# Kernel optimization log

Hardware: AMD Instinct MI355X
Metric: run time of the kernel (lower is better)

## Reference

```python
import jax, jax.numpy as jnp
import numpy as np
from math import pi

EPS = 1e-7
GAIN = 3.5  # weight_logits_softmax_gain
MAX_LOG_VAR = 3.5


def _upper_triangular(v, T, K, D):
    # replicate tf concat([v, v[...,::-1], zeros[...,D]], axis=2) -> reshape [T,K,D,D] -> strict-upper mask
    zero_pad = jnp.zeros((T, K, D), dtype=v.dtype)
    a_flat = jnp.concatenate([v, v[..., ::-1], zero_pad], axis=2)
    a = a_flat.reshape(T, K, D, D)
    idx = jnp.arange(D)
    mask = (idx[:, None] < idx[None, :]).astype(v.dtype)
    return a * mask[None, None, :, :]


def _diag_transforms(cov_param, T, K, D):
    ut = _upper_triangular(cov_param, T, K, D)
    a = 0.5 * (jnp.swapaxes(ut, -1, -2) - ut)  # antisymmetric [T,K,D,D]
    eye = jnp.eye(D, dtype=cov_param.dtype)[None, None]
    q = jnp.matmul(eye - a, jnp.linalg.inv(eye + a))  # Cayley transform
    return q


def setup_inputs() -> dict:
    key = jax.random.key(0)
    k1, k2, k3, k4, k5 = jax.random.split(key, 5)
    B, T, K, D = 2048, 512, 8, 8
    x = jax.random.normal(k1, (B, T, D), dtype=jnp.float32)
    kernel_centers = jax.random.uniform(k2, (T, K, D), dtype=jnp.float32)
    weight_logits = jax.random.normal(k3, (T, K), dtype=jnp.float32)
    log_variance = jax.random.normal(k4, (T, K, D), dtype=jnp.float32)
    cov_param = jax.random.normal(k5, (T, K, D * (D - 1) // 2), dtype=jnp.float32)
    return {"x": x, "kernel_centers": kernel_centers, "weight_logits": weight_logits,
            "log_variance": log_variance, "cov_param": cov_param}


def reference(x, kernel_centers, weight_logits, log_variance, cov_param):
    T, K, D = kernel_centers.shape
    # subtract kernel centers: [B,T,K,D]
    xc = x[:, :, None, :] - kernel_centers[None]
    # covariance-diagonalizing rotation (Cayley transform of antisym matrix)
    q = _diag_transforms(cov_param, T, K, D)  # [T,K,D,D]
    xt = jnp.einsum('btki,tkij->btkj', xc, q)
    # per-dimension Gaussian pdf
    var = jnp.exp(jnp.clip(log_variance, -MAX_LOG_VAR, MAX_LOG_VAR))[None]  # [1,T,K,D]
    norm_coeff = 1.0 / jnp.sqrt(2.0 * pi * var)
    gaussians = norm_coeff * jnp.exp(-0.5 * xt * xt / var)  # [B,T,K,D]
    # mix: product over dims (in log space), weighted sum over kernels
    lgpe = jnp.sum(jnp.log(gaussians + EPS), axis=-1)  # [B,T,K]
    p_kernels = jnp.exp(lgpe)
    w = jax.nn.softmax(jnp.clip(weight_logits, -GAIN, GAIN), axis=-1)  # [T,K]
    p = jnp.sum(p_kernels * w[None], axis=-1)  # [B,T]
    return p
```

## Files before the change

### kernel.cpp

```cpp
#include <hip/hip_runtime.h>
#include <math.h>

#define TDIM 512
#define KDIM 8
#define DDIM 8
#define BDIM 2048

#define PSTRIDE 80

#ifndef __has_builtin
#define __has_builtin(x) 0
#endif
#if __has_builtin(__builtin_amdgcn_exp2f)
#define FAST_EXP2(x) __builtin_amdgcn_exp2f(x)
#else
#define FAST_EXP2(x) exp2f(x)
#endif

__global__ __launch_bounds__(64) void precompute_kernel(
    const float* __restrict__ centers,
    const float* __restrict__ wlogits,
    const float* __restrict__ logvar,
    const float* __restrict__ covp,
    float* __restrict__ P,
    float* __restrict__ W)
{
    const int tid = blockIdx.x * 64 + threadIdx.x;

    float v[28];
    const float* vp = covp + (size_t)tid * 28;
    #pragma unroll
    for (int n = 0; n < 28; n++) v[n] = vp[n];

    double M[8][8];
    #pragma unroll
    for (int i = 0; i < 8; i++) {
        #pragma unroll
        for (int j = 0; j < 8; j++) {
            double a;
            if (i == j) {
                a = 0.0;
            } else if (i < j) {
                const int n = 8 * i + j;
                a = -0.5 * (double)((n < 28) ? v[n] : v[55 - n]);
            } else {
                const int n = 8 * j + i;
                a = 0.5 * (double)((n < 28) ? v[n] : v[55 - n]);
            }
            M[i][j] = (i == j ? 1.0 : 0.0) + a;
        }
    }

    #pragma unroll
    for (int c = 0; c < 8; c++) {
        const double p = 1.0 / M[c][c];
        M[c][c] = 1.0;
        #pragma unroll
        for (int j = 0; j < 8; j++) M[c][j] *= p;
        #pragma unroll
        for (int r = 0; r < 8; r++) {
            if (r == c) continue;
            const double f = M[r][c];
            M[r][c] = 0.0;
            #pragma unroll
            for (int j = 0; j < 8; j++) M[r][j] = fma(-f, M[c][j], M[r][j]);
        }
    }

    const float* lvp = logvar  + (size_t)tid * 8;
    const float* cp  = centers + (size_t)tid * 8;
    float* pk = P + (size_t)tid * PSTRIDE;

    const double SQ    = 0.84932180028801904;
    const double NORMC = 0.39894228040143268;

    #pragma unroll
    for (int j = 0; j < 8; j++) {
        double lv = (double)lvp[j];
        lv = fmin(fmax(lv, -3.5), 3.5);
        const double invstd = exp(-0.5 * lv);
        const double sc = invstd * SQ;
        double off = 0.0;
        #pragma unroll
        for (int i = 0; i < 8; i++) {
            const double q = 2.0 * M[i][j] - (i == j ? 1.0 : 0.0);
            const double r = q * sc;
            pk[j * 10 + i] = (float)r;
            off += (double)cp[i] * r;
        }
        pk[j * 10 + 8] = (float)off;
        pk[j * 10 + 9] = (float)(NORMC * invstd);
    }

    float l = wlogits[tid];
    l = fminf(fmaxf(l, -3.5f), 3.5f);
    float m = l;
    for (int o = 4; o >= 1; o >>= 1) m = fmaxf(m, __shfl_xor(m, o, 8));
    const float e = expf(l - m);
    float s = e;
    for (int o = 4; o >= 1; o >>= 1) s += __shfl_xor(s, o, 8);
    W[tid] = e / s;
}

__global__ __launch_bounds__(512, 4) void pecd_main_kernel(
    const float* __restrict__ x,
    const float* __restrict__ P,
    const float* __restrict__ W,
    float* __restrict__ out)
{
    __shared__ float xs[64 * 68];

    const int t0     = (int)blockIdx.x * 8;
    const int b_base = (int)blockIdx.y * 256;
    const int wave   = threadIdx.x >> 6;
    const int lane   = threadIdx.x & 63;

    const int t  = t0 + wave;
    const int ts = __builtin_amdgcn_readfirstlane(t);
    const float* __restrict__ Pt = P + (size_t)ts * (KDIM * PSTRIDE);
    const float* __restrict__ Wt = W + (size_t)ts * KDIM;

    float xv[4][8];
    #pragma unroll
    for (int c = 0; c < 4; c++) {
        const int b0 = b_base + c * 64;
        __syncthreads();
        #pragma unroll
        for (int it = 0; it < 2; it++) {
            const int idx = (int)threadIdx.x + it * 512;
            const int row = idx >> 4;
            const int col = idx & 15;
            const float4 val =
                *((const float4*)(x + ((size_t)(b0 + row) * TDIM + t0) * DDIM) + col);
            *(float4*)(xs + row * 68 + col * 4) = val;
        }
        __syncthreads();
        const float* xr = xs + lane * 68 + wave * 8;
        const float4 a0 = *(const float4*)(xr);
        const float4 a1 = *(const float4*)(xr + 4);
        xv[c][0] = a0.x; xv[c][1] = a0.y; xv[c][2] = a0.z; xv[c][3] = a0.w;
        xv[c][4] = a1.x; xv[c][5] = a1.y; xv[c][6] = a1.z; xv[c][7] = a1.w;
    }

    float acc[4] = {0.f, 0.f, 0.f, 0.f};
    #pragma unroll 1
    for (int k = 0; k < KDIM; k++) {
        const float* pk = Pt + k * PSTRIDE;
        const float wk = Wt[k];
        float prod[4] = {1.f, 1.f, 1.f, 1.f};
        #pragma unroll
        for (int j = 0; j < 8; j++) {
            float rr[10];
            #pragma unroll
            for (int q = 0; q < 10; q++) rr[q] = pk[j * 10 + q];
            #pragma unroll
            for (int c = 0; c < 4; c++) {
                float u = -rr[8];
                #pragma unroll
                for (int i = 0; i < 8; i++) u = fmaf(xv[c][i], rr[i], u);
                const float e = FAST_EXP2(-(u * u));
                prod[c] *= fmaf(rr[9], e, 1e-7f);
            }
        }
        #pragma unroll
        for (int c = 0; c < 4; c++) acc[c] = fmaf(wk, prod[c], acc[c]);
    }

    #pragma unroll
    for (int c = 0; c < 4; c++)
        out[(size_t)(b_base + c * 64 + lane) * TDIM + t] = acc[c];
}

extern "C" void kernel_launch(void* const* d_in, const int* in_sizes, int n_in,
                              void* d_out, int out_size, void* d_ws, size_t ws_size,
                              hipStream_t stream) {
    const float* x       = (const float*)d_in[0];
    const float* centers = (const float*)d_in[1];
    const float* wlogits = (const float*)d_in[2];
    const float* logvar  = (const float*)d_in[3];
    const float* covp    = (const float*)d_in[4];
    float* out = (float*)d_out;

    float* P = (float*)d_ws;
    float* W = P + (size_t)TDIM * KDIM * PSTRIDE;

    precompute_kernel<<<dim3(64), dim3(64), 0, stream>>>(
        centers, wlogits, logvar, covp, P, W);

    dim3 grid(TDIM / 8, BDIM / 256);
    pecd_main_kernel<<<grid, dim3(512), 0, stream>>>(x, P, W, out);
}
```

Measured before the change: 108.5 us.

## Fuse Cayley-transform precompute into main kernel with per-block shared parameters

Removes the separate precompute launch and computes the per-(t,k) rotation, scales, offsets and softmax weights inside each block, with 8 lanes cooperating per matrix in fp32 Gauss-Jordan via shuffles. Parameters are stored in LDS in a transposed layout read with float4 loads, instead of being fetched from global memory. This drops a kernel launch and the serial double-precision inversion, but every block along the batch axis now redoes the precompute, and lowering it from fp64 to fp32 may reduce accuracy.

```diff
diff --git a/kernel.cpp b/kernel.cpp
--- a/kernel.cpp
+++ b/kernel.cpp
@@ -5,8 +5,7 @@
 #define KDIM 8
 #define DDIM 8
 #define BDIM 2048
-
-#define PSTRIDE 80
+#define EPSF 1e-7f
 
 #ifndef __has_builtin
 #define __has_builtin(x) 0
@@ -17,108 +16,106 @@
 #define FAST_EXP2(x) exp2f(x)
 #endif
 
-__global__ __launch_bounds__(64) void precompute_kernel(
+__global__ __launch_bounds__(512, 4) void pecd_fused(
+    const float* __restrict__ x,
     const float* __restrict__ centers,
     const float* __restrict__ wlogits,
     const float* __restrict__ logvar,
     const float* __restrict__ covp,
-    float* __restrict__ P,
-    float* __restrict__ W)
+    float* __restrict__ out)
 {
-    const int tid = blockIdx.x * 64 + threadIdx.x;
+    __shared__ float prm[64 * 80];
+    __shared__ float Wl[64];
+    __shared__ float xs[64 * 68];
 
-    float v[28];
-    const float* vp = covp + (size_t)tid * 28;
-    #pragma unroll
-    for (int n = 0; n < 28; n++) v[n] = vp[n];
+    const int tidx   = (int)threadIdx.x;
+    const int t0     = (int)blockIdx.x * 8;
+    const int b_base = (int)blockIdx.y * 256;
 
-    double M[8][8];
-    #pragma unroll
-    for (int i = 0; i < 8; i++) {
+    {
+        const int tk = tidx >> 3;
+        const int r  = tidx & 7;
+        const int kk = tk & 7;
+        const int tl = tk >> 3;
+        const size_t tkg = (size_t)(t0 + tl) * 8 + kk;
+
+        const float* cb = covp + tkg * 28;
+        float row[8];
         #pragma unroll
         for (int j = 0; j < 8; j++) {
-            double a;
-            if (i == j) {
-                a = 0.0;
-            } else if (i < j) {
-                const int n = 8 * i + j;
-                a = -0.5 * (double)((n < 28) ? v[n] : v[55 - n]);
-            } else {
-                const int n = 8 * j + i;
-                a = 0.5 * (double)((n < 28) ? v[n] : v[55 - n]);
+            const int lo = (r < j) ? r : j;
+            const int hi = (r < j) ? j : r;
+            const int n  = 8 * lo + hi;
+            const int m  = (r == j) ? 0 : ((n < 28) ? n : 55 - n);
+            const float v = cb[m];
+            const float a = (r < j) ? -0.5f * v : 0.5f * v;
+            row[j] = (r == j) ? 1.0f : a;
+        }
+
+        #pragma unroll
+        for (int c = 0; c < 8; c++) {
+            float prow[8];
+            #pragma unroll
+            for (int j = 0; j < 8; j++) prow[j] = __shfl(row[j], c, 8);
+            const float pinv = 1.0f / prow[c];
+            const float f = row[c];
+            #pragma unroll
+            for (int j = 0; j < 8; j++) {
+                if (j == c) {
+                    row[j] = (r == c) ? pinv : -f * pinv;
+                } else {
+                    const float spiv = prow[j] * pinv;
+                    row[j] = (r == c) ? spiv : fmaf(-f, spiv, row[j]);
+                }
             }
-            M[i][j] = (i == j ? 1.0 : 0.0) + a;
         }
+
+        const float* lvp = logvar + tkg * 8;
+        float invstd[8];
+        #pragma unroll
+        for (int j = 0; j < 8; j++) {
+            const float lv = fminf(fmaxf(lvp[j], -3.5f), 3.5f);
+            invstd[j] = exp2f(lv * -0.7213475204444817f);
+        }
+        const float cr = centers[tkg * 8 + r];
+        float* pp = prm + tk * 80;
+        float offp[8];
+        #pragma unroll
+        for (int j = 0; j < 8; j++) {
+            const float q = 2.0f * row[j] - (r == j ? 1.0f : 0.0f);
+            const float val = q * (invstd[j] * 0.8493218002880191f);
+            pp[j * 8 + r] = val;
+            offp[j] = cr * val;
+        }
+        #pragma unroll
+        for (int j = 0; j < 8; j++) {
+            offp[j] += __shfl_xor(offp[j], 1, 8);
+            offp[j] += __shfl_xor(offp[j], 2, 8);
+            offp[j] += __shfl_xor(offp[j], 4, 8);
+        }
+        if (r == 0) {
+            #pragma unroll
+            for (int j = 0; j < 8; j++) {
+                pp[64 + j] = offp[j];
+                pp[72 + j] = 0.3989422804014327f * invstd[j];
+            }
+        }
+
+        float l = fminf(fmaxf(wlogits[tkg], -3.5f), 3.5f);
+        float mx = l;
+        mx = fmaxf(mx, __shfl_xor(mx, 8, 64));
+        mx = fmaxf(mx, __shfl_xor(mx, 16, 64));
+        mx = fmaxf(mx, __shfl_xor(mx, 32, 64));
+        const float e = exp2f((l - mx) * 1.4426950408889634f);
+        float ss = e;
+        ss += __shfl_xor(ss, 8, 64);
+        ss += __shfl_xor(ss, 16, 64);
+        ss += __shfl_xor(ss, 32, 64);
+        if (r == 0) Wl[tk] = e / ss;
     }
 
-    #pragma unroll
-    for (int c = 0; c < 8; c++) {
-        const double p = 1.0 / M[c][c];
-        M[c][c] = 1.0;
-        #pragma unroll
-        for (int j = 0; j < 8; j++) M[c][j] *= p;
-        #pragma unroll
-        for (int r = 0; r < 8; r++) {
-            if (r == c) continue;
-            const double f = M[r][c];
-            M[r][c] = 0.0;
-            #pragma unroll
-            for (int j = 0; j < 8; j++) M[r][j] = fma(-f, M[c][j], M[r][j]);
-        }
-    }
-
-    const float* lvp = logvar  + (size_t)tid * 8;
-    const float* cp  = centers + (size_t)tid * 8;
-    float* pk = P + (size_t)tid * PSTRIDE;
-
-    const double SQ    = 0.84932180028801904;
-    const double NORMC = 0.39894228040143268;
-
-    #pragma unroll
-    for (int j = 0; j < 8; j++) {
-        double lv = (double)lvp[j];
-        lv = fmin(fmax(lv, -3.5), 3.5);
-        const double invstd = exp(-0.5 * lv);
-        const double sc = invstd * SQ;
-        double off = 0.0;
-        #pragma unroll
-        for (int i = 0; i < 8; i++) {
-            const double q = 2.0 * M[i][j] - (i == j ? 1.0 : 0.0);
-            const double r = q * sc;
-            pk[j * 10 + i] = (float)r;
-            off += (double)cp[i] * r;
-        }
-        pk[j * 10 + 8] = (float)off;
-        pk[j * 10 + 9] = (float)(NORMC * invstd);
-    }
-
-    float l = wlogits[tid];
-    l = fminf(fmaxf(l, -3.5f), 3.5f);
-    float m = l;
-    for (int o = 4; o >= 1; o >>= 1) m = fmaxf(m, __shfl_xor(m, o, 8));
-    const float e = expf(l - m);
-    float s = e;
-    for (int o = 4; o >= 1; o >>= 1) s += __shfl_xor(s, o, 8);
-    W[tid] = e / s;
-}
-
-__global__ __launch_bounds__(512, 4) void pecd_main_kernel(
-    const float* __restrict__ x,
-    const float* __restrict__ P,
-    const float* __restrict__ W,
-    float* __restrict__ out)
-{
-    __shared__ float xs[64 * 68];
-
-    const int t0     = (int)blockIdx.x * 8;
-    const int b_base = (int)blockIdx.y * 256;
-    const int wave   = threadIdx.x >> 6;
-    const int lane   = threadIdx.x & 63;
-
-    const int t  = t0 + wave;
-    const int ts = __builtin_amdgcn_readfirstlane(t);
-    const float* __restrict__ Pt = P + (size_t)ts * (KDIM * PSTRIDE);
-    const float* __restrict__ Wt = W + (size_t)ts * KDIM;
+    const int wave = tidx >> 6;
+    const int lane = tidx & 63;
 
     float xv[4][8];
     #pragma unroll
@@ -127,12 +124,12 @@
         __syncthreads();
         #pragma unroll
         for (int it = 0; it < 2; it++) {
-            const int idx = (int)threadIdx.x + it * 512;
-            const int row = idx >> 4;
-            const int col = idx & 15;
+            const int idx  = tidx + it * 512;
+            const int brow = idx >> 4;
+            const int col  = idx & 15;
             const float4 val =
-                *((const float4*)(x + ((size_t)(b0 + row) * TDIM + t0) * DDIM) + col);
-            *(float4*)(xs + row * 68 + col * 4) = val;
+                *((const float4*)(x + ((size_t)(b0 + brow) * TDIM + t0) * DDIM) + col);
+            *(float4*)(xs + brow * 68 + col * 4) = val;
         }
         __syncthreads();
         const float* xr = xs + lane * 68 + wave * 8;
@@ -142,24 +139,30 @@
         xv[c][4] = a1.x; xv[c][5] = a1.y; xv[c][6] = a1.z; xv[c][7] = a1.w;
     }
 
+    const float* pw = prm + wave * (8 * 80);
     float acc[4] = {0.f, 0.f, 0.f, 0.f};
     #pragma unroll 1
     for (int k = 0; k < KDIM; k++) {
-        const float* pk = Pt + k * PSTRIDE;
-        const float wk = Wt[k];
+        const float* pk = pw + k * 80;
+        float off[8], nc[8];
+        *(float4*)&off[0] = *(const float4*)(pk + 64);
+        *(float4*)&off[4] = *(const float4*)(pk + 68);
+        *(float4*)&nc[0]  = *(const float4*)(pk + 72);
+        *(float4*)&nc[4]  = *(const float4*)(pk + 76);
+        const float wk = Wl[wave * 8 + k];
         float prod[4] = {1.f, 1.f, 1.f, 1.f};
         #pragma unroll
         for (int j = 0; j < 8; j++) {
-            float rr[10];
-            #pragma unroll
-            for (int q = 0; q < 10; q++) rr[q] = pk[j * 10 + q];
+            float rr[8];
+            *(float4*)&rr[0] = *(const float4*)(pk + j * 8);
+            *(float4*)&rr[4] = *(const float4*)(pk + j * 8 + 4);
             #pragma unroll
             for (int c = 0; c < 4; c++) {
-                float u = -rr[8];
+                float u = -off[j];
                 #pragma unroll
                 for (int i = 0; i < 8; i++) u = fmaf(xv[c][i], rr[i], u);
-                const float e = FAST_EXP2(-(u * u));
-                prod[c] *= fmaf(rr[9], e, 1e-7f);
+                const float e2 = FAST_EXP2(-(u * u));
+                prod[c] *= fmaf(nc[j], e2, EPSF);
             }
         }
         #pragma unroll
@@ -168,7 +171,7 @@
 
     #pragma unroll
     for (int c = 0; c < 4; c++)
-        out[(size_t)(b_base + c * 64 + lane) * TDIM + t] = acc[c];
+        out[(size_t)(b_base + c * 64 + lane) * TDIM + (t0 + wave)] = acc[c];
 }
 
 extern "C" void kernel_launch(void* const* d_in, const int* in_sizes, int n_in,
@@ -180,13 +183,8 @@
     const float* logvar  = (const float*)d_in[3];
     const float* covp    = (const float*)d_in[4];
     float* out = (float*)d_out;
-
-    float* P = (float*)d_ws;
-    float* W = P + (size_t)TDIM * KDIM * PSTRIDE;
-
-    precompute_kernel<<<dim3(64), dim3(64), 0, stream>>>(
-        centers, wlogits, logvar, covp, P, W);
+    (void)d_ws; (void)ws_size;
 
     dim3 grid(TDIM / 8, BDIM / 256);
-    pecd_main_kernel<<<grid, dim3(512), 0, stream>>>(x, P, W, out);
+    pecd_fused<<<grid, dim3(512), 0, stream>>>(x, centers, wlogits, logvar, covp, out);
 }
```

Result: faster. 104.0 us (-4.2%).
